# Kernel optimization log

Measured on AMD Instinct MI355X. Metric: run time of the kernel, lower is better.

The kernel has to match this reference:

```python
import jax, jax.numpy as jnp
import numpy as np

B = 512          # number of (query, corpus) pairs
MAX_SET = 128    # max_set_size
D_IN, E_IN = 32, 16
D = 128          # node_state_dim == filters_3
E_ENC = 64
M_HID = 256
T_DIM = 128      # transform_dim
N_PROP = 5
SINKHORN_ITERS = 20
TEMP = 0.1
DEG = 8


def setup_inputs() -> dict:
    key = jax.random.key(0)
    ks = jax.random.split(key, 16)
    # alternating graph sizes: query 128/64, corpus 64/128
    qsizes = np.where(np.arange(B) % 2 == 0, 128, 64).astype(np.int32)
    csizes = np.where(np.arange(B) % 2 == 0, 64, 128).astype(np.int32)
    sizes_flat = np.stack([qsizes, csizes], 1).reshape(-1)        # [2B] interleaved q,c
    N = int(sizes_flat.sum())                                     # 98304
    E = DEG * N                                                   # 786432
    starts = np.concatenate([[0], np.cumsum(sizes_flat)[:-1]])
    graph_idx = np.repeat(np.arange(2 * B), sizes_flat).astype(np.int32)
    rng = np.random.default_rng(0)
    from_idx = rng.integers(0, N, E).astype(np.int64)
    g = graph_idx[from_idx]                                       # keep edges within a graph
    to_idx = (starts[g] + rng.integers(0, 1 << 30, E) % sizes_flat[g]).astype(np.int64)

    def W(k, shape):
        s = 1.0 / np.sqrt(shape[0])
        return jax.random.uniform(k, shape, jnp.float32, -s, s)

    return dict(
        node_features=jax.random.normal(ks[0], (N, D_IN), jnp.float32),
        edge_features=jax.random.normal(ks[1], (E, E_IN), jnp.float32),
        enc_node_w=W(ks[2], (D_IN, D)), enc_node_b=jnp.zeros((D,), jnp.float32),
        enc_edge_w=W(ks[3], (E_IN, E_ENC)), enc_edge_b=jnp.zeros((E_ENC,), jnp.float32),
        msg_w1=W(ks[4], (2 * D + E_ENC, M_HID)), msg_b1=jnp.zeros((M_HID,), jnp.float32),
        msg_w2=W(ks[5], (M_HID, D)), msg_b2=jnp.zeros((D,), jnp.float32),
        rmsg_w1=W(ks[6], (2 * D + E_ENC, M_HID)), rmsg_b1=jnp.zeros((M_HID,), jnp.float32),
        rmsg_w2=W(ks[7], (M_HID, D)), rmsg_b2=jnp.zeros((D,), jnp.float32),
        upd_w1=W(ks[8], (2 * D, M_HID)), upd_b1=jnp.zeros((M_HID,), jnp.float32),
        upd_w2=W(ks[9], (M_HID, D)), upd_b2=jnp.zeros((D,), jnp.float32),
        fc1_w=W(ks[10], (D, T_DIM)), fc1_b=jnp.zeros((T_DIM,), jnp.float32),
        fc2_w=W(ks[11], (T_DIM, T_DIM)), fc2_b=jnp.zeros((T_DIM,), jnp.float32),
        from_idx=jnp.asarray(from_idx, jnp.int32),
        to_idx=jnp.asarray(to_idx, jnp.int32),
        graph_idx=jnp.asarray(graph_idx, jnp.int32),
        qsizes=jnp.asarray(qsizes, jnp.int32),
        csizes=jnp.asarray(csizes, jnp.int32),
    )


def _mlp2(x, w1, b1, w2, b2):
    return jax.nn.relu(x @ w1 + b1) @ w2 + b2


def reference(node_features, edge_features, enc_node_w, enc_node_b, enc_edge_w, enc_edge_b,
              msg_w1, msg_b1, msg_w2, msg_b2, rmsg_w1, rmsg_b1, rmsg_w2, rmsg_b2,
              upd_w1, upd_b1, upd_w2, upd_b2, fc1_w, fc1_b, fc2_w, fc2_b,
              from_idx, to_idx, graph_idx, qsizes, csizes):
    N = node_features.shape[0]
    # GraphEncoder: linear MLPs on node / edge features
    h = node_features @ enc_node_w + enc_node_b                   # [N, D]
    e = edge_features @ enc_edge_w + enc_edge_b                   # [E, E_ENC]
    # GraphPropLayer applied n_prop_layers times (shared params)
    for _ in range(N_PROP):
        src, dst = h[from_idx], h[to_idx]
        m = _mlp2(jnp.concatenate([src, dst, e], -1), msg_w1, msg_b1, msg_w2, msg_b2)
        agg = jax.ops.segment_sum(m, to_idx, num_segments=N)
        mr = _mlp2(jnp.concatenate([dst, src, e], -1), rmsg_w1, rmsg_b1, rmsg_w2, rmsg_b2)
        agg = agg + jax.ops.segment_sum(mr, from_idx, num_segments=N)
        h = h + _mlp2(jnp.concatenate([agg, h], -1), upd_w1, upd_b1, upd_w2, upd_b2)
    # split into per-graph chunks and pad to MAX_SET (scatter by (pair, side, position))
    sizes_flat = jnp.stack([qsizes, csizes], 1).reshape(-1)       # [2B]
    starts = jnp.concatenate([jnp.zeros((1,), sizes_flat.dtype), jnp.cumsum(sizes_flat)[:-1]])
    pos = jnp.arange(N, dtype=jnp.int32) - starts[graph_idx]
    pair, side = graph_idx // 2, graph_idx % 2
    stacked = jnp.zeros((B, 2, MAX_SET, D), h.dtype).at[pair, side, pos].set(h)
    stacked_q, stacked_c = stacked[:, 0], stacked[:, 1]           # [B, MAX_SET, D]
    # masked transform
    tq = _mlp2(stacked_q, fc1_w, fc1_b, fc2_w, fc2_b)
    tc = _mlp2(stacked_c, fc1_w, fc1_b, fc2_w, fc2_b)
    ar = jnp.arange(MAX_SET)
    qmask = (ar[None, :] < qsizes[:, None]).astype(h.dtype)[:, :, None]
    cmask = (ar[None, :] < csizes[:, None]).astype(h.dtype)[:, :, None]
    mq, mc = qmask * tq, cmask * tc
    # sinkhorn (noise_factor = 0, temperature = 0.1, 20 iters)
    log_alpha = jnp.einsum('bqd,bcd->bqc', mq, mc) / TEMP         # [B, MAX_SET, MAX_SET]
    for _ in range(SINKHORN_ITERS):
        log_alpha = log_alpha - jax.scipy.special.logsumexp(log_alpha, axis=2, keepdims=True)
        log_alpha = log_alpha - jax.scipy.special.logsumexp(log_alpha, axis=1, keepdims=True)
    plan = jnp.exp(log_alpha)
    # masked residual score
    scores = -jnp.sum(jax.nn.relu(stacked_q - plan @ stacked_c), axis=(1, 2))  # [B]
    return scores
```

## Files before the change

### kernel.cpp

```cpp
#include <hip/hip_runtime.h>

using bf16x8 = __attribute__((ext_vector_type(8))) __bf16;
using u16x8  = __attribute__((ext_vector_type(8))) unsigned short;
using f32x4  = __attribute__((ext_vector_type(4))) float;
using f32x2  = __attribute__((ext_vector_type(2))) float;

#define DEV static __device__ __forceinline__

constexpr int NN = 98304;
constexpr int NE = 786432;
constexpr int NB = 512;

constexpr size_t OFF_HB  = 0;
constexpr size_t OFF_AGG = OFF_HB + (size_t)NN*128*2;
constexpr size_t OFF_TH  = OFF_AGG;
constexpr size_t OFF_TL  = OFF_AGG + (size_t)NN*128*2;
constexpr size_t OFF_W   = OFF_AGG + (size_t)NN*128*4;

constexpr size_t WO_W1TM = 0;
constexpr size_t WO_W1TR = WO_W1TM + (size_t)81920*2;
constexpr size_t WO_W2TM = WO_W1TR + (size_t)81920*2;
constexpr size_t WO_W2TR = WO_W2TM + (size_t)32768*2;
constexpr size_t WO_W1TU = WO_W2TR + (size_t)32768*2;
constexpr size_t WO_W2TU = WO_W1TU + (size_t)65536*2;
constexpr size_t WO_WNT  = WO_W2TU + (size_t)32768*2;
constexpr size_t WO_WETP = WO_WNT  + (size_t)4096*2;
constexpr size_t WO_FC1F = WO_WETP + (size_t)2048*2;
constexpr size_t WO_FC2F = WO_FC1F + (size_t)16384*4;
constexpr size_t WO_BNF  = WO_FC2F + (size_t)16384*4;
constexpr size_t WO_BEF  = WO_BNF + 128*4;
constexpr size_t WO_B1M  = WO_BEF + 64*4;
constexpr size_t WO_B2M  = WO_B1M + 256*4;
constexpr size_t WO_B1R  = WO_B2M + 128*4;
constexpr size_t WO_B2R  = WO_B1R + 256*4;
constexpr size_t WO_B1U  = WO_B2R + 128*4;
constexpr size_t WO_B2U  = WO_B1U + 256*4;
constexpr size_t WO_FC1B = WO_B2U + 128*4;
constexpr size_t WO_FC2B = WO_FC1B + 128*4;
constexpr size_t WO_FLAG = WO_FC2B + 128*4;
constexpr size_t WO_END  = WO_FLAG + 16;

constexpr size_t OFF_HL  = OFF_W + WO_END;
constexpr size_t WS_MINI = OFF_HL;
constexpr size_t WS_FULL = OFF_HL + (size_t)NN*128*2;

constexpr int    SCAN_CHUNKS= NN/256;
constexpr size_t CSR_INTS   = (size_t)2*(NN+1) + (size_t)2*NN + (size_t)2*NE + 768;
constexpr size_t CSR_BYTES  = CSR_INTS*4;
constexpr size_t WS_FULL_G  = WS_FULL + CSR_BYTES;
constexpr size_t WS_MINI_G  = WS_MINI + CSR_BYTES;

DEV unsigned short f2bf(float f){
  unsigned u = __float_as_uint(f);
  u += 0x7fffu + ((u >> 16) & 1u);
  return (unsigned short)(u >> 16);
}
DEV float bf2f(unsigned short s){ return __uint_as_float(((unsigned)s) << 16); }

DEV unsigned short ldbf(const void* p, size_t i, int fl){
  return fl ? ((const unsigned short*)p)[i] : f2bf(((const float*)p)[i]);
}
DEV float ldf(const void* p, size_t i, int fl){
  return fl ? bf2f(((const unsigned short*)p)[i]) : ((const float*)p)[i];
}

DEV f32x4 mfma16(u16x8 a, u16x8 b, f32x4 c){
  bf16x8 A, B;
  __builtin_memcpy(&A, &a, 16);
  __builtin_memcpy(&B, &b, 16);
  return __builtin_amdgcn_mfma_f32_16x16x32_bf16(A, B, c, 0, 0, 0);
}

__global__ void k_dtype(const unsigned short* nf_u16, int* flag){
  if (threadIdx.x != 0 || blockIdx.x != 0) return;
  int sane = 0;
  for (int i = 0; i < 64; ++i){
    unsigned short v = nf_u16[2*i];
    int e = (v >> 7) & 0xFF;
    if (e >= 0x70 && e <= 0x8E) sane++;
  }
  *flag = (sane >= 32) ? 1 : 0;
}

__global__ void k_sent(float* out){
  int i = blockIdx.x*256 + threadIdx.x;
  if (i < NB) out[i] = 10000.f;
}

__global__ void k_canary(void* out, const int* flag){
  int i = blockIdx.x*256 + threadIdx.x;
  if (i < NB){
    if (*flag) ((unsigned short*)out)[i] = (unsigned short)0x4580u;
    else       ((float*)out)[i] = 4096.f;
  }
}

__global__ void k_zero(float* agg){
  f32x4* p = (f32x4*)agg;
  int gtid = blockIdx.x*256 + threadIdx.x;
  for (int i = gtid; i < NN*128/4; i += 786432){
    f32x4 z = {0.f, 0.f, 0.f, 0.f};
    p[i] = z;
  }
}

__global__ void k_prep(
  const void* enc_node_w, const void* enc_node_b,
  const void* enc_edge_w, const void* enc_edge_b,
  const void* msg_w1, const void* msg_b1,
  const void* msg_w2, const void* msg_b2,
  const void* rmsg_w1, const void* rmsg_b1,
  const void* rmsg_w2, const void* rmsg_b2,
  const void* upd_w1, const void* upd_b1,
  const void* upd_w2, const void* upd_b2,
  const void* fc1_w, const void* fc1_b,
  const void* fc2_w, const void* fc2_b,
  char* wsb)
{
  int fl = *(const int*)(wsb + OFF_W + WO_FLAG);
  int i = blockIdx.x*256 + threadIdx.x;
  unsigned short* W1Tm = (unsigned short*)(wsb + OFF_W + WO_W1TM);
  unsigned short* W1Tr = (unsigned short*)(wsb + OFF_W + WO_W1TR);
  unsigned short* W2Tm = (unsigned short*)(wsb + OFF_W + WO_W2TM);
  unsigned short* W2Tr = (unsigned short*)(wsb + OFF_W + WO_W2TR);
  unsigned short* W1Tu = (unsigned short*)(wsb + OFF_W + WO_W1TU);
  unsigned short* W2Tu = (unsigned short*)(wsb + OFF_W + WO_W2TU);
  unsigned short* WnT  = (unsigned short*)(wsb + OFF_W + WO_WNT);
  unsigned short* WeTp = (unsigned short*)(wsb + OFF_W + WO_WETP);
  float* fc1f = (float*)(wsb + OFF_W + WO_FC1F);
  float* fc2f = (float*)(wsb + OFF_W + WO_FC2F);
  float* bnf  = (float*)(wsb + OFF_W + WO_BNF);
  float* bef  = (float*)(wsb + OFF_W + WO_BEF);
  float* b1m  = (float*)(wsb + OFF_W + WO_B1M);
  float* b2m  = (float*)(wsb + OFF_W + WO_B2M);
  float* b1r  = (float*)(wsb + OFF_W + WO_B1R);
  float* b2r  = (float*)(wsb + OFF_W + WO_B2R);
  float* b1u  = (float*)(wsb + OFF_W + WO_B1U);
  float* b2u  = (float*)(wsb + OFF_W + WO_B2U);
  float* f1b  = (float*)(wsb + OFF_W + WO_FC1B);
  float* f2b  = (float*)(wsb + OFF_W + WO_FC2B);

  if (i < 81920){ W1Tm[i] = ldbf(msg_w1,  (size_t)(i%320)*256 + (i/320), fl); return; } i -= 81920;
  if (i < 81920){ W1Tr[i] = ldbf(rmsg_w1, (size_t)(i%320)*256 + (i/320), fl); return; } i -= 81920;
  if (i < 32768){ W2Tm[i] = ldbf(msg_w2,  (size_t)(i%256)*128 + (i/256), fl); return; } i -= 32768;
  if (i < 32768){ W2Tr[i] = ldbf(rmsg_w2, (size_t)(i%256)*128 + (i/256), fl); return; } i -= 32768;
  if (i < 65536){ W1Tu[i] = ldbf(upd_w1,  (size_t)(i%256)*256 + (i/256), fl); return; } i -= 65536;
  if (i < 32768){ W2Tu[i] = ldbf(upd_w2,  (size_t)(i%256)*128 + (i/256), fl); return; } i -= 32768;
  if (i <  4096){ WnT[i]  = ldbf(enc_node_w, (size_t)(i%32)*128 + (i/32), fl); return; } i -= 4096;
  if (i <  2048){ int k = i%32, n = i/32;
                  WeTp[i] = (k<16) ? ldbf(enc_edge_w, (size_t)k*64 + n, fl) : (unsigned short)0; return; } i -= 2048;
  if (i < 16384){ fc1f[i] = ldf(fc1_w, i, fl); return; } i -= 16384;
  if (i < 16384){ fc2f[i] = ldf(fc2_w, i, fl); return; } i -= 16384;
  if (i <   128){ bnf[i] = ldf(enc_node_b, i, fl); return; } i -= 128;
  if (i <    64){ bef[i] = ldf(enc_edge_b, i, fl); return; } i -= 64;
  if (i <   256){ b1m[i] = ldf(msg_b1, i, fl); return; } i -= 256;
  if (i <   128){ b2m[i] = ldf(msg_b2, i, fl); return; } i -= 128;
  if (i <   256){ b1r[i] = ldf(rmsg_b1, i, fl); return; } i -= 256;
  if (i <   128){ b2r[i] = ldf(rmsg_b2, i, fl); return; } i -= 128;
  if (i <   256){ b1u[i] = ldf(upd_b1, i, fl); return; } i -= 256;
  if (i <   128){ b2u[i] = ldf(upd_b2, i, fl); return; } i -= 128;
  if (i <   128){ f1b[i] = ldf(fc1_b, i, fl); return; } i -= 128;
  if (i <   128){ f2b[i] = ldf(fc2_b, i, fl); return; }
}

__global__ void k_csr_zero(int* cur0, int* cur1){
  int i = blockIdx.x*256 + threadIdx.x;
  if (i < NN){ cur0[i] = 0; cur1[i] = 0; }
}
__global__ void k_csr_count(const int* from_idx, const int* to_idx, int* cur0, int* cur1){
  int e = blockIdx.x*256 + threadIdx.x;
  if (e < NE){
    atomicAdd(&cur0[to_idx[e]], 1);
    atomicAdd(&cur1[from_idx[e]], 1);
  }
}
__global__ void k_scan1(const int* cur0, const int* cur1, int* csum){
  __shared__ int red[256];
  int b = blockIdx.x, tid = threadIdx.x;
  const int* c = (b >= SCAN_CHUNKS) ? cur1 : cur0;
  int cb = (b >= SCAN_CHUNKS) ? (b - SCAN_CHUNKS) : b;
  red[tid] = c[cb*256 + tid];
  __syncthreads();
  for (int off = 128; off > 0; off >>= 1){
    if (tid < off) red[tid] += red[tid + off];
    __syncthreads();
  }
  if (tid == 0) csum[b] = red[0];
}
__global__ void k_scan2(int* csum, int* offs0, int* offs1){
  int wv = threadIdx.x >> 6, lane = threadIdx.x & 63;
  if (wv >= 2) return;
  int basei = wv * SCAN_CHUNKS;
  int carry = 0;
  for (int j = 0; j < SCAN_CHUNKS/64; ++j){
    int x = csum[basei + j*64 + lane];
    int s = x;
    for (int off = 1; off < 64; off <<= 1){
      int t = __shfl_up(s, off, 64);
      if (lane >= off) s += t;
    }
    csum[basei + j*64 + lane] = s - x + carry;
    carry += __shfl(s, 63, 64);
  }
  if (lane == 0){
    if (wv == 0) offs0[NN] = carry; else offs1[NN] = carry;
  }
}
__global__ void k_scan3(int* cur0, int* cur1, const int* csum, int* offs0, int* offs1){
  __shared__ int s[256];
  int b = blockIdx.x, tid = threadIdx.x;
  int dir = (b >= SCAN_CHUNKS) ? 1 : 0;
  int cb  = dir ? (b - SCAN_CHUNKS) : b;
  int* c    = dir ? cur1 : cur0;
  int* offs = dir ? offs1 : offs0;
  int v = c[cb*256 + tid];
  s[tid] = v;
  __syncthreads();
  for (int off = 1; off < 256; off <<= 1){
    int t = (tid >= off) ? s[tid - off] : 0;
    __syncthreads();
    s[tid] += t;
    __syncthreads();
  }
  int excl = s[tid] - v + csum[b];
  offs[cb*256 + tid] = excl;
  c[cb*256 + tid] = excl;
}
__global__ void k_csr_fill(const int* from_idx, const int* to_idx,
                           int* cur0, int* cur1, int* ent0, int* ent1){
  int e = blockIdx.x*256 + threadIdx.x;
  if (e < NE){
    int p0 = atomicAdd(&cur0[to_idx[e]], 1);   ent0[p0] = e;
    int p1 = atomicAdd(&cur1[from_idx[e]], 1); ent1[p1] = e;
  }
}

__global__ void __launch_bounds__(256) k_enc_node(
  const void* nf, const unsigned short* wnt, const float* bnf,
  unsigned short* hb, unsigned short* hl, int has_hl, const int* flag)
{
  int fl = *flag;
  const u16x8* wnt8 = (const u16x8*)wnt;
  int tid = threadIdx.x, wv = tid>>6, lane = tid&63, quad = lane>>4, l15 = lane&15;
  int n0 = blockIdx.x*64;
  f32x4 acc[4][2];
  for (int a=0;a<4;a++){ f32x4 z = {0.f,0.f,0.f,0.f}; acc[a][0]=z; acc[a][1]=z; }
  u16x8 av[4], bv[2];
  if (fl){
    const u16x8* nf8 = (const u16x8*)nf;
    for (int mt=0; mt<4; ++mt) av[mt] = nf8[(size_t)(n0 + mt*16 + l15)*4 + quad];
  } else {
    const float* nff = (const float*)nf;
    for (int mt=0; mt<4; ++mt){
      const float* rp = nff + (size_t)(n0 + mt*16 + l15)*32 + quad*8;
      u16x8 v;
      for (int j=0;j<8;j++) v[j] = f2bf(rp[j]);
      av[mt] = v;
    }
  }
  for (int nt=0; nt<2; ++nt) bv[nt] = wnt8[(size_t)(wv*32 + nt*16 + l15)*4 + quad];
  for (int mt=0; mt<4; ++mt)
    for (int nt=0; nt<2; ++nt)
      acc[mt][nt] = mfma16(av[mt], bv[nt], acc[mt][nt]);
  for (int mt=0; mt<4; ++mt)
    for (int nt=0; nt<2; ++nt){
      int n = wv*32 + nt*16 + l15;
      float bias = bnf[n];
      for (int r=0;r<4;r++){
        int m = mt*16 + quad*4 + r;
        float v = acc[mt][nt][r] + bias;
        size_t idx = (size_t)(n0+m)*128 + n;
        unsigned short hi = f2bf(v);
        hb[idx] = hi;
        if (has_hl) hl[idx] = f2bf(v - bf2f(hi));
      }
    }
}

__global__ void __launch_bounds__(256) k_msg(
  const unsigned short* hbg, const void* efg,
  const int* from_idx, const int* to_idx,
  const unsigned short* w1tm, const unsigned short* w1tr,
  const unsigned short* w2tm, const unsigned short* w2tr,
  const unsigned short* wetp, const float* bef,
  const float* b1m, const float* b2m, const float* b1r, const float* b2r,
  float* agg, const int* flag)
{
  __shared__ __align__(16) unsigned short XsB[40*32*8];
  __shared__ __align__(16) unsigned short HsB[32*32*8];
  __shared__ int fromS[32], toS[32];
  int fl = *flag;
  u16x8* Xs = (u16x8*)XsB;
  u16x8* Hs = (u16x8*)HsB;
  const u16x8* hb8   = (const u16x8*)hbg;
  const u16x8* wetp8 = (const u16x8*)wetp;
  const u16x8* w1tm8 = (const u16x8*)w1tm;
  const u16x8* w1tr8 = (const u16x8*)w1tr;
  const u16x8* w2tm8 = (const u16x8*)w2tm;
  const u16x8* w2tr8 = (const u16x8*)w2tr;

  int tid = threadIdx.x;
  int e0 = blockIdx.x*32;
  if (tid < 32) fromS[tid] = from_idx[e0 + tid];
  else if (tid < 64) toS[tid-32] = to_idx[e0 + tid - 32];
  __syncthreads();
  int m = tid & 31, g = tid >> 5;
  int wv = tid>>6, lane = tid&63, quad = lane>>4, l15 = lane&15;
  u16x8 zero8 = {0,0,0,0,0,0,0,0};

  for (int j=0; j<4; ++j){
    int kb = g + 8*j;
    u16x8 v = (kb < 16) ? hb8[(size_t)fromS[m]*16 + kb]
                        : hb8[(size_t)toS[m]*16 + (kb-16)];
    Xs[kb*32 + m] = v;
  }
  {
    f32x4 accE[2];
    for (int a=0;a<2;a++){ f32x4 z = {0.f,0.f,0.f,0.f}; accE[a]=z; }
    u16x8 bvE = wetp8[(size_t)(wv*16 + l15)*4 + quad];
    for (int mt=0; mt<2; ++mt){
      u16x8 avE = zero8;
      if (quad < 2){
        if (fl){
          avE = ((const u16x8*)efg)[(size_t)(e0 + mt*16 + l15)*2 + quad];
        } else {
          const float* ep = (const float*)efg + (size_t)(e0 + mt*16 + l15)*16 + quad*8;
          u16x8 v;
          for (int j=0;j<8;j++) v[j] = f2bf(ep[j]);
          avE = v;
        }
      }
      accE[mt] = mfma16(avE, bvE, accE[mt]);
    }
    int n = wv*16 + l15;
    float bias = bef[n];
    for (int mt=0; mt<2; ++mt)
      for (int r=0;r<4;r++){
        int me = mt*16 + quad*4 + r;
        XsB[((32 + (n>>3))*32 + me)*8 + (n&7)] = f2bf(accE[mt][r] + bias);
      }
  }
  __syncthreads();

  for (int dir=0; dir<2; ++dir){
    const u16x8* W1T = dir ? w1tr8 : w1tm8;
    const u16x8* W2T = dir ? w2tr8 : w2tm8;
    const float* B1  = dir ? b1r : b1m;
    const float* B2  = dir ? b2r : b2m;
    f32x4 acc1[2][4];
    for (int a=0;a<2;a++)
      for (int b=0;b<4;b++){ f32x4 z = {0.f,0.f,0.f,0.f}; acc1[a][b]=z; }
    for (int ks=0; ks<10; ++ks){
      u16x8 bv[4], av[2];
      for (int nt=0; nt<4; ++nt)
        bv[nt] = W1T[(size_t)(wv*64 + nt*16 + l15)*40 + ks*4 + quad];
      int kb = ks*4 + quad;
      int kbm = dir ? (kb < 32 ? (kb ^ 16) : kb) : kb;
      for (int mt=0; mt<2; ++mt)
        av[mt] = Xs[kbm*32 + mt*16 + l15];
      for (int mt=0; mt<2; ++mt)
        for (int nt=0; nt<4; ++nt)
          acc1[mt][nt] = mfma16(av[mt], bv[nt], acc1[mt][nt]);
    }
    __syncthreads();
    for (int mt=0; mt<2; ++mt)
      for (int nt=0; nt<4; ++nt){
        int n = wv*64 + nt*16 + l15;
        float bias = B1[n];
        for (int r=0;r<4;r++){
          int mm = mt*16 + quad*4 + r;
          float v = fmaxf(acc1[mt][nt][r] + bias, 0.f);
          HsB[((n>>3)*32 + mm)*8 + (n&7)] = f2bf(v);
        }
      }
    __syncthreads();
    f32x4 acc2[2][2];
    for (int a=0;a<2;a++)
      for (int b=0;b<2;b++){ f32x4 z = {0.f,0.f,0.f,0.f}; acc2[a][b]=z; }
    for (int ks=0; ks<8; ++ks){
      u16x8 bv[2], av[2];
      for (int nt=0; nt<2; ++nt)
        bv[nt] = W2T[(size_t)(wv*32 + nt*16 + l15)*32 + ks*4 + quad];
      for (int mt=0; mt<2; ++mt)
        av[mt] = Hs[(ks*4 + quad)*32 + mt*16 + l15];
      for (int mt=0; mt<2; ++mt)
        for (int nt=0; nt<2; ++nt)
          acc2[mt][nt] = mfma16(av[mt], bv[nt], acc2[mt][nt]);
    }
    for (int mt=0; mt<2; ++mt)
      for (int nt=0; nt<2; ++nt){
        int n = wv*32 + nt*16 + l15;
        float bias = B2[n];
        for (int r=0;r<4;r++){
          int mm = mt*16 + quad*4 + r;
          int row = dir ? fromS[mm] : toS[mm];
          atomicAdd(agg + (size_t)row*128 + n, acc2[mt][nt][r] + bias);
        }
      }
  }
}

__global__ void __launch_bounds__(1024, 4) k_msg9(
  const unsigned short* hbg, const void* efg,
  const int* from_idx, const int* to_idx, const int* ent,
  const unsigned short* w1tm, const unsigned short* w1tr,
  const unsigned short* w2tm, const unsigned short* w2tr,
  const unsigned short* wetp, const float* bef,
  const float* b1m, const float* b2m, const float* b1r, const float* b2r,
  float* agg, const int* flag)
{
  __shared__ __align__(16) unsigned short XsB[40*128*8];
  __shared__ __align__(16) unsigned short HsB[32*128*8];
  __shared__ int eS[128], fromS[128], toS[128];
  __shared__ int runBeg[129];
  __shared__ int nRunsS;
  int fl = *flag;
  u16x8* Xs = (u16x8*)XsB;
  u16x8* Hs = (u16x8*)HsB;
  const u16x8* hb8   = (const u16x8*)hbg;
  const u16x8* wetp8 = (const u16x8*)wetp;
  const u16x8* w1tm8 = (const u16x8*)w1tm;
  const u16x8* w1tr8 = (const u16x8*)w1tr;
  const u16x8* w2tm8 = (const u16x8*)w2tm;
  const u16x8* w2tr8 = (const u16x8*)w2tr;

  int tid = threadIdx.x;
  int cpx = (int)gridDim.x >> 3;
  int bb = ((int)blockIdx.x & 7) * cpx + ((int)blockIdx.x >> 3);
  int e0 = bb * 128;
  if (tid < 128){
    int e = ent[e0 + tid];
    eS[tid] = e;
    fromS[tid] = from_idx[e];
    toS[tid]   = to_idx[e];
  }
  __syncthreads();
  int w = tid>>6, lane = tid&63, quad = lane>>4, l15 = lane&15;
  u16x8 zero8 = {0,0,0,0,0,0,0,0};

  if (tid == 0){
    int nr = 0;
    for (int mm=0; mm<128; ++mm)
      if (mm==0 || toS[mm]!=toS[mm-1]) runBeg[nr++] = mm;
    runBeg[nr] = 128; nRunsS = nr;
  }
  {
    int edge = tid & 127, cg = tid >> 7;
    for (int j=0; j<4; ++j){
      int kb = cg + 8*j;
      u16x8 v = (kb < 16) ? hb8[(size_t)fromS[edge]*16 + kb]
                          : hb8[(size_t)toS[edge]*16 + (kb-16)];
      Xs[kb*128 + edge] = v;
    }
  }
  {
    int wm = w >> 2, wn = w & 3;
    f32x4 accE[2];
    for (int a=0;a<2;a++){ f32x4 z = {0.f,0.f,0.f,0.f}; accE[a]=z; }
    u16x8 bvE = wetp8[(size_t)(wn*16 + l15)*4 + quad];
    for (int mt=0; mt<2; ++mt){
      u16x8 avE = zero8;
      if (quad < 2){
        int e = eS[wm*32 + mt*16 + l15];
        if (fl){
          avE = ((const u16x8*)efg)[(size_t)e*2 + quad];
        } else {
          const float* ep = (const float*)efg + (size_t)e*16 + quad*8;
          u16x8 v;
          for (int j=0;j<8;j++) v[j] = f2bf(ep[j]);
          avE = v;
        }
      }
      accE[mt] = mfma16(avE, bvE, accE[mt]);
    }
    int n = wn*16 + l15;
    float bias = bef[n];
    for (int mt=0; mt<2; ++mt)
      for (int r=0;r<4;r++){
        int me = wm*32 + mt*16 + quad*4 + r;
        XsB[((32 + (n>>3))*128 + me)*8 + (n&7)] = f2bf(accE[mt][r] + bias);
      }
  }
  __syncthreads();

  for (int dir=0; dir<2; ++dir){
    const u16x8* W1T = dir ? w1tr8 : w1tm8;
    const u16x8* W2T = dir ? w2tr8 : w2tm8;
    const float* B1  = dir ? b1r : b1m;
    f32x4 acc1[8];
    for (int a=0;a<8;a++){ f32x4 z = {0.f,0.f,0.f,0.f}; acc1[a]=z; }
    int n1 = w*16 + l15;
    for (int ks=0; ks<10; ++ks){
      u16x8 bv1 = W1T[(size_t)n1*40 + ks*4 + quad];
      int kb = ks*4 + quad;
      int kbm = dir ? (kb < 32 ? (kb ^ 16) : kb) : kb;
      u16x8 av[8];
      for (int mt=0; mt<8; ++mt)
        av[mt] = Xs[kbm*128 + mt*16 + l15];
      for (int mt=0; mt<8; ++mt)
        acc1[mt] = mfma16(av[mt], bv1, acc1[mt]);
    }
    if (dir == 1) __syncthreads();
    {
      float bias1 = B1[n1];
      for (int mt=0; mt<8; ++mt)
        for (int r=0;r<4;r++){
          int mm = mt*16 + quad*4 + r;
          float v = fmaxf(acc1[mt][r] + bias1, 0.f);
          HsB[((n1>>3)*128 + mm)*8 + (n1&7)] = f2bf(v);
        }
    }
    __syncthreads();
    int wm2 = w >> 3, wn2 = w & 7;
    int n2 = wn2*16 + l15;
    f32x4 acc2[4];
    for (int a=0;a<4;a++){ f32x4 z = {0.f,0.f,0.f,0.f}; acc2[a]=z; }
    for (int ks=0; ks<8; ++ks){
      u16x8 bv2 = W2T[(size_t)n2*32 + ks*4 + quad];
      u16x8 av[4];
      for (int mt=0; mt<4; ++mt)
        av[mt] = Hs[(ks*4 + quad)*128 + wm2*64 + mt*16 + l15];
      for (int mt=0; mt<4; ++mt)
        acc2[mt] = mfma16(av[mt], bv2, acc2[mt]);
    }
    if (dir == 0){
      __syncthreads();
      float* P = (float*)HsB;
      float bias = b2m[n2];
      for (int mt=0; mt<4; ++mt)
        for (int r=0;r<4;r++){
          int mm = wm2*64 + mt*16 + quad*4 + r;
          P[mm*128 + n2] = acc2[mt][r] + bias;
        }
      __syncthreads();
      int col = tid & 127, grp = tid >> 7;
      int nr = nRunsS;
      for (int k = grp; k < nr; k += 8){
        int r0 = runBeg[k], r1 = runBeg[k+1];
        float s = 0.f;
        for (int mm = r0; mm < r1; ++mm) s += P[mm*128 + col];
        atomicAdd(agg + (size_t)toS[r0]*128 + col, s);
      }
    } else {
      float bias = b2r[n2];
      for (int mt=0; mt<4; ++mt)
        for (int r=0;r<4;r++){
          int mm = wm2*64 + mt*16 + quad*4 + r;
          atomicAdd(agg + (size_t)fromS[mm]*128 + n2, acc2[mt][r] + bias);
        }
    }
  }
}

__global__ void __launch_bounds__(512, 4) k_upd(
  const float* agg, const unsigned short* hbg,
  const unsigned short* w1tu, const unsigned short* w2tu,
  const float* b1u, const float* b2u,
  unsigned short* hb, unsigned short* hl, int has_hl)
{
  __shared__ __align__(16) unsigned short XsB[32*64*8];
  __shared__ __align__(16) unsigned short HsB[32*64*8];
  u16x8* Xs = (u16x8*)XsB;
  u16x8* Hs = (u16x8*)HsB;
  const u16x8* hb8   = (const u16x8*)hbg;
  const u16x8* w1tu8 = (const u16x8*)w1tu;
  const u16x8* w2tu8 = (const u16x8*)w2tu;
  int tid = threadIdx.x;
  int n0 = blockIdx.x*64;
  {
    int node = tid & 63, cg = tid >> 6;
    for (int j=0; j<4; ++j){
      int kb = cg + 8*j;
      u16x8 v;
      if (kb < 16){
        const float* ap = agg + (size_t)(n0+node)*128 + kb*8;
        for (int t=0;t<8;t++) v[t] = f2bf(ap[t]);
      } else {
        v = hb8[(size_t)(n0+node)*16 + (kb-16)];
      }
      Xs[kb*64 + node] = v;
    }
  }
  __syncthreads();
  int w = tid>>6, lane = tid&63, quad = lane>>4, l15 = lane&15;
  f32x4 acc1[4][2];
  for (int a=0;a<4;a++)
    for (int b=0;b<2;b++){ f32x4 z = {0.f,0.f,0.f,0.f}; acc1[a][b]=z; }
  for (int ks=0; ks<8; ++ks){
    u16x8 bv[2], av[4];
    for (int nt=0; nt<2; ++nt)
      bv[nt] = w1tu8[(size_t)(w*32 + nt*16 + l15)*32 + ks*4 + quad];
    for (int mt=0; mt<4; ++mt)
      av[mt] = Xs[(ks*4 + quad)*64 + mt*16 + l15];
    for (int mt=0; mt<4; ++mt)
      for (int nt=0; nt<2; ++nt)
        acc1[mt][nt] = mfma16(av[mt], bv[nt], acc1[mt][nt]);
  }
  __syncthreads();
  for (int mt=0; mt<4; ++mt)
    for (int nt=0; nt<2; ++nt){
      int n = w*32 + nt*16 + l15;
      float bias = b1u[n];
      for (int r=0;r<4;r++){
        int mm = mt*16 + quad*4 + r;
        float v = fmaxf(acc1[mt][nt][r] + bias, 0.f);
        HsB[((n>>3)*64 + mm)*8 + (n&7)] = f2bf(v);
      }
    }
  __syncthreads();
  f32x4 acc2[4];
  for (int a=0;a<4;a++){ f32x4 z = {0.f,0.f,0.f,0.f}; acc2[a]=z; }
  int n2 = w*16 + l15;
  for (int ks=0; ks<8; ++ks){
    u16x8 bv2 = w2tu8[(size_t)n2*32 + ks*4 + quad];
    u16x8 av[4];
    for (int mt=0; mt<4; ++mt)
      av[mt] = Hs[(ks*4 + quad)*64 + mt*16 + l15];
    for (int mt=0; mt<4; ++mt)
      acc2[mt] = mfma16(av[mt], bv2, acc2[mt]);
  }
  float bias = b2u[n2];
  for (int mt=0; mt<4; ++mt)
    for (int r=0;r<4;r++){
      int mm = mt*16 + quad*4 + r;
      size_t idx = (size_t)(n0+mm)*128 + n2;
      float base = bf2f(hb[idx]);
      if (has_hl) base += bf2f(hl[idx]);
      float nv = base + acc2[mt][r] + bias;
      unsigned short hi = f2bf(nv);
      hb[idx] = hi;
      if (has_hl) hl[idx] = f2bf(nv - bf2f(hi));
    }
}

__global__ void __launch_bounds__(256) k_tmlp(
  const unsigned short* hb, const unsigned short* hl, int has_hl,
  const float* fc1f, const float* fc2f,
  const float* fc1b, const float* fc2b, unsigned short* Th, unsigned short* Tl)
{
  __shared__ float Xs[16][128];
  __shared__ float Hsm[16][128];
  int tid = threadIdx.x, wv = tid>>6, lane = tid&63;
  int nodeBase = blockIdx.x*16 + wv*4;
  for (int i=0;i<4;i++){
    size_t base = (size_t)(nodeBase+i)*128 + lane*2;
    float x0 = bf2f(hb[base]), x1 = bf2f(hb[base+1]);
    if (has_hl){ x0 += bf2f(hl[base]); x1 += bf2f(hl[base+1]); }
    Xs[wv*4+i][lane*2] = x0; Xs[wv*4+i][lane*2+1] = x1;
  }
  __syncthreads();
  float a0[4], a1[4];
  for (int i=0;i<4;i++){ a0[i] = fc1b[lane*2]; a1[i] = fc1b[lane*2+1]; }
  for (int k=0;k<128;k++){
    f32x2 w = *(const f32x2*)&fc1f[k*128 + lane*2];
    for (int i=0;i<4;i++){ float x = Xs[wv*4+i][k]; a0[i] += x*w[0]; a1[i] += x*w[1]; }
  }
  for (int i=0;i<4;i++){
    Hsm[wv*4+i][lane*2]   = fmaxf(a0[i], 0.f);
    Hsm[wv*4+i][lane*2+1] = fmaxf(a1[i], 0.f);
  }
  __syncthreads();
  for (int i=0;i<4;i++){ a0[i] = fc2b[lane*2]; a1[i] = fc2b[lane*2+1]; }
  for (int k=0;k<128;k++){
    f32x2 w = *(const f32x2*)&fc2f[k*128 + lane*2];
    for (int i=0;i<4;i++){ float x = Hsm[wv*4+i][k]; a0[i] += x*w[0]; a1[i] += x*w[1]; }
  }
  for (int i=0;i<4;i++){
    size_t idx = (size_t)(nodeBase+i)*128 + lane*2;
    float t0 = a0[i], t1 = a1[i];
    unsigned short h0 = f2bf(t0), h1 = f2bf(t1);
    Th[idx] = h0; Th[idx+1] = h1;
    Tl[idx]   = f2bf(t0 - bf2f(h0));
    Tl[idx+1] = f2bf(t1 - bf2f(h1));
  }
}

__global__ void __launch_bounds__(256) k_pair(
  const unsigned short* Th, const unsigned short* Tl,
  const unsigned short* hb, const unsigned short* hl, int has_hl,
  void* outv, const int* flag)
{
  __shared__ float la[8448];
  __shared__ float red[4];
  const u16x8* th8 = (const u16x8*)Th;
  const u16x8* tl8 = (const u16x8*)Tl;
  int b = blockIdx.x;
  int even = ((b & 1) == 0);
  int qs = even ? 128 : 64;
  int cs = 192 - qs;
  int nr = even ? 128 : 65;
  int nc = even ? 65 : 128;
  int st = nc + 1;
  int q0 = 192*b, c0 = q0 + qs;
  int tid = threadIdx.x, wv = tid>>6, lane = tid&63, quad = lane>>4, l15 = lane&15;
  u16x8 zero8 = {0,0,0,0,0,0,0,0};

  f32x4 acc[2][8];
  for (int a=0;a<2;a++)
    for (int c=0;c<8;c++){ f32x4 z = {0.f,0.f,0.f,0.f}; acc[a][c]=z; }
  for (int pass=0; pass<3; ++pass){
    const u16x8* A  = (pass==2) ? tl8 : th8;
    const u16x8* Bm = (pass==1) ? tl8 : th8;
    for (int ks=0; ks<4; ++ks){
      u16x8 av[2], bv[8];
      for (int mt=0; mt<2; ++mt){
        int q = wv*32 + mt*16 + l15;
        av[mt] = (q < qs) ? A[(size_t)(q0+q)*16 + ks*4 + quad] : zero8;
      }
      for (int nt=0; nt<8; ++nt){
        int c = nt*16 + l15;
        bv[nt] = (c < cs) ? Bm[(size_t)(c0+c)*16 + ks*4 + quad] : zero8;
      }
      for (int mt=0; mt<2; ++mt)
        for (int nt=0; nt<8; ++nt)
          acc[mt][nt] = mfma16(av[mt], bv[nt], acc[mt][nt]);
    }
  }
  for (int mt=0; mt<2; ++mt)
    for (int nt=0; nt<8; ++nt)
      for (int r=0;r<4;r++){
        int q = wv*32 + mt*16 + quad*4 + r;
        int c = nt*16 + l15;
        if (q < nr && c < nc) la[q*st + c] = acc[mt][nt][r] * 10.0f;
      }
  __syncthreads();

  for (int it=0; it<20; ++it){
    if (tid < nr){
      float* row = &la[tid*st];
      float mx = -1e30f;
      for (int c=0;c<nc;c++) mx = fmaxf(mx, row[c]);
      float s = 0.f, last = 0.f;
      for (int c=0;c<nc;c++){ float e = __expf(row[c]-mx); s += e; last = e; }
      if (even) s += 63.f * last;
      float l = mx + __logf(s);
      for (int c=0;c<nc;c++) row[c] -= l;
    }
    __syncthreads();
    if (tid < nc){
      int c = tid;
      float mx = -1e30f;
      for (int r=0;r<nr;r++) mx = fmaxf(mx, la[r*st + c]);
      float s = 0.f, last = 0.f;
      for (int r=0;r<nr;r++){ float e = __expf(la[r*st + c]-mx); s += e; last = e; }
      if (!even) s += 63.f * last;
      float l = mx + __logf(s);
      for (int r=0;r<nr;r++) la[r*st + c] -= l;
    }
    __syncthreads();
  }
  for (int i = tid; i < 8448; i += 256) la[i] = __expf(la[i]);
  __syncthreads();

  int d = tid & 127, qg = tid >> 7;
  int nsweep = (nr + 15) >> 4;
  float partial = 0.f;
  for (int sweep=0; sweep<nsweep; ++sweep){
    int qb = sweep*16 + qg*8;
    float acc2[8];
    for (int j=0;j<8;j++) acc2[j] = 0.f;
    for (int c=0; c<cs; ++c){
      size_t si = (size_t)(c0+c)*128 + d;
      float s = bf2f(hb[si]);
      if (has_hl) s += bf2f(hl[si]);
      for (int j=0;j<8;j++){
        int r = qb + j;
        if (r < nr) acc2[j] += la[r*st + c] * s;
      }
    }
    for (int j=0;j<8;j++){
      int r = qb + j;
      if (r < nr){
        float w = (!even && r == 64) ? 64.f : 1.f;
        float sq = 0.f;
        if (r < qs){
          size_t si = (size_t)(q0+r)*128 + d;
          sq = bf2f(hb[si]);
          if (has_hl) sq += bf2f(hl[si]);
        }
        partial += w * fmaxf(sq - acc2[j], 0.f);
      }
    }
  }
  for (int off=32; off>0; off>>=1) partial += __shfl_down(partial, off, 64);
  if (lane == 0) red[wv] = partial;
  __syncthreads();
  if (tid == 0){
    float tot = red[0] + red[1] + red[2] + red[3];
    if (*flag) ((unsigned short*)outv)[b] = f2bf(-tot);
    else       ((float*)outv)[b] = -tot;
  }
}

extern "C" void kernel_launch(void* const* d_in, const int* in_sizes, int n_in,
                              void* d_out, int out_size, void* d_ws, size_t ws_size,
                              hipStream_t stream)
{
  if (ws_size < WS_MINI){
    k_sent<<<2, 256, 0, stream>>>((float*)d_out);
    return;
  }
  int has_hl = 0, use_s9 = 0;
  size_t off_csr = 0;
  if (ws_size >= WS_FULL_G){ has_hl = 1; use_s9 = 1; off_csr = WS_FULL; }
  else if (ws_size >= WS_FULL){ has_hl = 1; use_s9 = 0; }
  else if (ws_size >= WS_MINI_G){ has_hl = 0; use_s9 = 1; off_csr = WS_MINI; }

  const int* from_idx = (const int*)d_in[22];
  const int* to_idx   = (const int*)d_in[23];

  char* wsb = (char*)d_ws;
  unsigned short* hb  = (unsigned short*)(wsb + OFF_HB);
  unsigned short* hl  = (unsigned short*)(wsb + OFF_HL);
  float* agg          = (float*)(wsb + OFF_AGG);
  unsigned short* Th  = (unsigned short*)(wsb + OFF_TH);
  unsigned short* Tl  = (unsigned short*)(wsb + OFF_TL);
  int* flag           = (int*)(wsb + OFF_W + WO_FLAG);

  const unsigned short* w1tm = (const unsigned short*)(wsb + OFF_W + WO_W1TM);
  const unsigned short* w1tr = (const unsigned short*)(wsb + OFF_W + WO_W1TR);
  const unsigned short* w2tm = (const unsigned short*)(wsb + OFF_W + WO_W2TM);
  const unsigned short* w2tr = (const unsigned short*)(wsb + OFF_W + WO_W2TR);
  const unsigned short* w1tu = (const unsigned short*)(wsb + OFF_W + WO_W1TU);
  const unsigned short* w2tu = (const unsigned short*)(wsb + OFF_W + WO_W2TU);
  const unsigned short* wnt  = (const unsigned short*)(wsb + OFF_W + WO_WNT);
  const unsigned short* wetp = (const unsigned short*)(wsb + OFF_W + WO_WETP);
  const float* fc1f  = (const float*)(wsb + OFF_W + WO_FC1F);
  const float* fc2f  = (const float*)(wsb + OFF_W + WO_FC2F);
  const float* bnf   = (const float*)(wsb + OFF_W + WO_BNF);
  const float* bef   = (const float*)(wsb + OFF_W + WO_BEF);
  const float* b1m   = (const float*)(wsb + OFF_W + WO_B1M);
  const float* b2m   = (const float*)(wsb + OFF_W + WO_B2M);
  const float* b1r   = (const float*)(wsb + OFF_W + WO_B1R);
  const float* b2r   = (const float*)(wsb + OFF_W + WO_B2R);
  const float* b1u   = (const float*)(wsb + OFF_W + WO_B1U);
  const float* b2u   = (const float*)(wsb + OFF_W + WO_B2U);
  const float* f1b   = (const float*)(wsb + OFF_W + WO_FC1B);
  const float* f2b   = (const float*)(wsb + OFF_W + WO_FC2B);

  int* offs0 = (int*)(wsb + off_csr);
  int* offs1 = offs0 + (NN + 1);
  int* cur0  = offs1 + (NN + 1);
  int* cur1  = cur0 + NN;
  int* ent0  = cur1 + NN;
  int* ent1  = ent0 + NE;
  int* csum  = ent1 + NE;

  k_dtype<<<1, 64, 0, stream>>>((const unsigned short*)d_in[0], flag);

  k_canary<<<2, 256, 0, stream>>>(d_out, flag);

  k_prep<<<1439, 256, 0, stream>>>(
    d_in[2],  d_in[3],  d_in[4],  d_in[5],
    d_in[6],  d_in[7],  d_in[8],  d_in[9],
    d_in[10], d_in[11], d_in[12], d_in[13],
    d_in[14], d_in[15], d_in[16], d_in[17],
    d_in[18], d_in[19], d_in[20], d_in[21],
    wsb);

  if (use_s9){
    k_csr_zero <<<NN/256, 256, 0, stream>>>(cur0, cur1);
    k_csr_count<<<NE/256, 256, 0, stream>>>(from_idx, to_idx, cur0, cur1);
    k_scan1    <<<2*SCAN_CHUNKS, 256, 0, stream>>>(cur0, cur1, csum);
    k_scan2    <<<1, 128, 0, stream>>>(csum, offs0, offs1);
    k_scan3    <<<2*SCAN_CHUNKS, 256, 0, stream>>>(cur0, cur1, csum, offs0, offs1);
    k_csr_fill <<<NE/256, 256, 0, stream>>>(from_idx, to_idx, cur0, cur1, ent0, ent1);
  }

  k_enc_node<<<NN/64, 256, 0, stream>>>(d_in[0], wnt, bnf, hb, hl, has_hl, flag);

  for (int r=0; r<5; ++r){
    k_zero<<<3072, 256, 0, stream>>>(agg);
    if (use_s9){
      k_msg9<<<NE/128, 1024, 0, stream>>>(hb, d_in[1],
          from_idx, to_idx, ent0, w1tm, w1tr, w2tm, w2tr, wetp, bef,
          b1m, b2m, b1r, b2r, agg, flag);
    } else {
      k_msg<<<NE/32, 256, 0, stream>>>(hb, d_in[1],
          from_idx, to_idx, w1tm, w1tr, w2tm, w2tr, wetp, bef,
          b1m, b2m, b1r, b2r, agg, flag);
    }
    k_upd<<<NN/64, 512, 0, stream>>>(agg, hb, w1tu, w2tu, b1u, b2u, hb, hl, has_hl);
  }

  k_tmlp<<<NN/16, 256, 0, stream>>>(hb, hl, has_hl, fc1f, fc2f, f1b, f2b, Th, Tl);
  k_pair<<<NB, 256, 0, stream>>>(Th, Tl, hb, hl, has_hl, d_out, flag);
}
```

Baseline: 6.004 ms.

## Shrink message kernel tile to 64 edges, prefetch weights, fuse agg zeroing into update

The message kernel now processes 64 edges per 512-thread block instead of 128 per 1024-thread block. Each wave computes a 32-column slice of the first GEMM, which halves LDS use and allows more resident blocks. The weight B-fragments in the message and update GEMMs are register double-buffered, loading the next k-step while the current MFMAs issue. The per-round k_zero launch is dropped: k_upd clears its own agg rows after reading them, so only one initial zero pass remains. The trade-offs are larger edge-segment run overhead from smaller tiles and more atomics per edge group, and the in-place zeroing relies on each block owning its agg rows.

```diff
diff --git a/kernel.cpp b/kernel.cpp
--- a/kernel.cpp
+++ b/kernel.cpp
@@ -400,7 +400,7 @@
   }
 }
 
-__global__ void __launch_bounds__(1024, 4) k_msg9(
+__global__ void __launch_bounds__(512, 4) k_msg8(
   const unsigned short* hbg, const void* efg,
   const int* from_idx, const int* to_idx, const int* ent,
   const unsigned short* w1tm, const unsigned short* w1tr,
@@ -409,10 +409,10 @@
   const float* b1m, const float* b2m, const float* b1r, const float* b2r,
   float* agg, const int* flag)
 {
-  __shared__ __align__(16) unsigned short XsB[40*128*8];
-  __shared__ __align__(16) unsigned short HsB[32*128*8];
-  __shared__ int eS[128], fromS[128], toS[128];
-  __shared__ int runBeg[129];
+  __shared__ __align__(16) unsigned short XsB[40*64*8];
+  __shared__ __align__(16) unsigned short HsB[32*64*8];
+  __shared__ int eS[64], fromS[64], toS[64];
+  __shared__ int runBeg[65];
   __shared__ int nRunsS;
   int fl = *flag;
   u16x8* Xs = (u16x8*)XsB;
@@ -427,8 +427,8 @@
   int tid = threadIdx.x;
   int cpx = (int)gridDim.x >> 3;
   int bb = ((int)blockIdx.x & 7) * cpx + ((int)blockIdx.x >> 3);
-  int e0 = bb * 128;
-  if (tid < 128){
+  int e0 = bb * 64;
+  if (tid < 64){
     int e = ent[e0 + tid];
     eS[tid] = e;
     fromS[tid] = from_idx[e];
@@ -440,17 +440,17 @@
 
   if (tid == 0){
     int nr = 0;
-    for (int mm=0; mm<128; ++mm)
+    for (int mm=0; mm<64; ++mm)
       if (mm==0 || toS[mm]!=toS[mm-1]) runBeg[nr++] = mm;
-    runBeg[nr] = 128; nRunsS = nr;
+    runBeg[nr] = 64; nRunsS = nr;
   }
   {
-    int edge = tid & 127, cg = tid >> 7;
+    int edge = tid & 63, cg = tid >> 6;
     for (int j=0; j<4; ++j){
       int kb = cg + 8*j;
       u16x8 v = (kb < 16) ? hb8[(size_t)fromS[edge]*16 + kb]
                           : hb8[(size_t)toS[edge]*16 + (kb-16)];
-      Xs[kb*128 + edge] = v;
+      Xs[kb*64 + edge] = v;
     }
   }
   {
@@ -478,7 +478,7 @@
     for (int mt=0; mt<2; ++mt)
       for (int r=0;r<4;r++){
         int me = wm*32 + mt*16 + quad*4 + r;
-        XsB[((32 + (n>>3))*128 + me)*8 + (n&7)] = f2bf(accE[mt][r] + bias);
+        XsB[((32 + (n>>3))*64 + me)*8 + (n&7)] = f2bf(accE[mt][r] + bias);
       }
   }
   __syncthreads();
@@ -487,41 +487,52 @@
     const u16x8* W1T = dir ? w1tr8 : w1tm8;
     const u16x8* W2T = dir ? w2tr8 : w2tm8;
     const float* B1  = dir ? b1r : b1m;
-    f32x4 acc1[8];
-    for (int a=0;a<8;a++){ f32x4 z = {0.f,0.f,0.f,0.f}; acc1[a]=z; }
-    int n1 = w*16 + l15;
+    f32x4 acc1[4][2];
+    for (int a=0;a<4;a++)
+      for (int b=0;b<2;b++){ f32x4 z = {0.f,0.f,0.f,0.f}; acc1[a][b]=z; }
+    u16x8 bvA[2], bvB[2];
+    for (int nt=0; nt<2; ++nt)
+      bvA[nt] = W1T[(size_t)(w*32 + nt*16 + l15)*40 + quad];
     for (int ks=0; ks<10; ++ks){
-      u16x8 bv1 = W1T[(size_t)n1*40 + ks*4 + quad];
+      if (ks < 9)
+        for (int nt=0; nt<2; ++nt)
+          bvB[nt] = W1T[(size_t)(w*32 + nt*16 + l15)*40 + (ks+1)*4 + quad];
+      else { bvB[0] = bvA[0]; bvB[1] = bvA[1]; }
       int kb = ks*4 + quad;
       int kbm = dir ? (kb < 32 ? (kb ^ 16) : kb) : kb;
-      u16x8 av[8];
-      for (int mt=0; mt<8; ++mt)
-        av[mt] = Xs[kbm*128 + mt*16 + l15];
-      for (int mt=0; mt<8; ++mt)
-        acc1[mt] = mfma16(av[mt], bv1, acc1[mt]);
+      u16x8 av[4];
+      for (int mt=0; mt<4; ++mt)
+        av[mt] = Xs[kbm*64 + mt*16 + l15];
+      for (int mt=0; mt<4; ++mt)
+        for (int nt=0; nt<2; ++nt)
+          acc1[mt][nt] = mfma16(av[mt], bvA[nt], acc1[mt][nt]);
+      bvA[0] = bvB[0]; bvA[1] = bvB[1];
     }
     if (dir == 1) __syncthreads();
-    {
-      float bias1 = B1[n1];
-      for (int mt=0; mt<8; ++mt)
+    for (int mt=0; mt<4; ++mt)
+      for (int nt=0; nt<2; ++nt){
+        int n = w*32 + nt*16 + l15;
+        float bias = B1[n];
         for (int r=0;r<4;r++){
           int mm = mt*16 + quad*4 + r;
-          float v = fmaxf(acc1[mt][r] + bias1, 0.f);
-          HsB[((n1>>3)*128 + mm)*8 + (n1&7)] = f2bf(v);
+          float v = fmaxf(acc1[mt][nt][r] + bias, 0.f);
+          HsB[((n>>3)*64 + mm)*8 + (n&7)] = f2bf(v);
         }
-    }
+      }
     __syncthreads();
-    int wm2 = w >> 3, wn2 = w & 7;
-    int n2 = wn2*16 + l15;
     f32x4 acc2[4];
     for (int a=0;a<4;a++){ f32x4 z = {0.f,0.f,0.f,0.f}; acc2[a]=z; }
+    int n2 = w*16 + l15;
+    u16x8 bvC = W2T[(size_t)n2*32 + quad];
     for (int ks=0; ks<8; ++ks){
-      u16x8 bv2 = W2T[(size_t)n2*32 + ks*4 + quad];
+      u16x8 bvN = bvC;
+      if (ks < 7) bvN = W2T[(size_t)n2*32 + (ks+1)*4 + quad];
       u16x8 av[4];
       for (int mt=0; mt<4; ++mt)
-        av[mt] = Hs[(ks*4 + quad)*128 + wm2*64 + mt*16 + l15];
+        av[mt] = Hs[(ks*4 + quad)*64 + mt*16 + l15];
       for (int mt=0; mt<4; ++mt)
-        acc2[mt] = mfma16(av[mt], bv2, acc2[mt]);
+        acc2[mt] = mfma16(av[mt], bvC, acc2[mt]);
+      bvC = bvN;
     }
     if (dir == 0){
       __syncthreads();
@@ -529,13 +540,13 @@
       float bias = b2m[n2];
       for (int mt=0; mt<4; ++mt)
         for (int r=0;r<4;r++){
-          int mm = wm2*64 + mt*16 + quad*4 + r;
+          int mm = mt*16 + quad*4 + r;
           P[mm*128 + n2] = acc2[mt][r] + bias;
         }
       __syncthreads();
       int col = tid & 127, grp = tid >> 7;
       int nr = nRunsS;
-      for (int k = grp; k < nr; k += 8){
+      for (int k = grp; k < nr; k += 4){
         int r0 = runBeg[k], r1 = runBeg[k+1];
         float s = 0.f;
         for (int mm = r0; mm < r1; ++mm) s += P[mm*128 + col];
@@ -545,7 +556,7 @@
       float bias = b2r[n2];
       for (int mt=0; mt<4; ++mt)
         for (int r=0;r<4;r++){
-          int mm = wm2*64 + mt*16 + quad*4 + r;
+          int mm = mt*16 + quad*4 + r;
           atomicAdd(agg + (size_t)fromS[mm]*128 + n2, acc2[mt][r] + bias);
         }
     }
@@ -553,7 +564,7 @@
 }
 
 __global__ void __launch_bounds__(512, 4) k_upd(
-  const float* agg, const unsigned short* hbg,
+  float* agg, const unsigned short* hbg,
   const unsigned short* w1tu, const unsigned short* w2tu,
   const float* b1u, const float* b2u,
   unsigned short* hb, unsigned short* hl, int has_hl)
@@ -582,19 +593,32 @@
     }
   }
   __syncthreads();
+  {
+    f32x4* ap4 = (f32x4*)(agg + (size_t)n0*128);
+    f32x4 z = {0.f,0.f,0.f,0.f};
+    for (int i = tid; i < 64*128/4; i += 512) ap4[i] = z;
+  }
   int w = tid>>6, lane = tid&63, quad = lane>>4, l15 = lane&15;
   f32x4 acc1[4][2];
   for (int a=0;a<4;a++)
     for (int b=0;b<2;b++){ f32x4 z = {0.f,0.f,0.f,0.f}; acc1[a][b]=z; }
-  for (int ks=0; ks<8; ++ks){
-    u16x8 bv[2], av[4];
+  {
+    u16x8 bvA[2], bvB[2];
     for (int nt=0; nt<2; ++nt)
-      bv[nt] = w1tu8[(size_t)(w*32 + nt*16 + l15)*32 + ks*4 + quad];
-    for (int mt=0; mt<4; ++mt)
-      av[mt] = Xs[(ks*4 + quad)*64 + mt*16 + l15];
-    for (int mt=0; mt<4; ++mt)
-      for (int nt=0; nt<2; ++nt)
-        acc1[mt][nt] = mfma16(av[mt], bv[nt], acc1[mt][nt]);
+      bvA[nt] = w1tu8[(size_t)(w*32 + nt*16 + l15)*32 + quad];
+    for (int ks=0; ks<8; ++ks){
+      if (ks < 7)
+        for (int nt=0; nt<2; ++nt)
+          bvB[nt] = w1tu8[(size_t)(w*32 + nt*16 + l15)*32 + (ks+1)*4 + quad];
+      else { bvB[0] = bvA[0]; bvB[1] = bvA[1]; }
+      u16x8 av[4];
+      for (int mt=0; mt<4; ++mt)
+        av[mt] = Xs[(ks*4 + quad)*64 + mt*16 + l15];
+      for (int mt=0; mt<4; ++mt)
+        for (int nt=0; nt<2; ++nt)
+          acc1[mt][nt] = mfma16(av[mt], bvA[nt], acc1[mt][nt]);
+      bvA[0] = bvB[0]; bvA[1] = bvB[1];
+    }
   }
   __syncthreads();
   for (int mt=0; mt<4; ++mt)
@@ -611,13 +635,18 @@
   f32x4 acc2[4];
   for (int a=0;a<4;a++){ f32x4 z = {0.f,0.f,0.f,0.f}; acc2[a]=z; }
   int n2 = w*16 + l15;
-  for (int ks=0; ks<8; ++ks){
-    u16x8 bv2 = w2tu8[(size_t)n2*32 + ks*4 + quad];
-    u16x8 av[4];
-    for (int mt=0; mt<4; ++mt)
-      av[mt] = Hs[(ks*4 + quad)*64 + mt*16 + l15];
-    for (int mt=0; mt<4; ++mt)
-      acc2[mt] = mfma16(av[mt], bv2, acc2[mt]);
+  {
+    u16x8 bvC = w2tu8[(size_t)n2*32 + quad];
+    for (int ks=0; ks<8; ++ks){
+      u16x8 bvN = bvC;
+      if (ks < 7) bvN = w2tu8[(size_t)n2*32 + (ks+1)*4 + quad];
+      u16x8 av[4];
+      for (int mt=0; mt<4; ++mt)
+        av[mt] = Hs[(ks*4 + quad)*64 + mt*16 + l15];
+      for (int mt=0; mt<4; ++mt)
+        acc2[mt] = mfma16(av[mt], bvC, acc2[mt]);
+      bvC = bvN;
+    }
   }
   float bias = b2u[n2];
   for (int mt=0; mt<4; ++mt)
@@ -800,11 +829,11 @@
     k_sent<<<2, 256, 0, stream>>>((float*)d_out);
     return;
   }
-  int has_hl = 0, use_s9 = 0;
+  int has_hl = 0, use_s8 = 0;
   size_t off_csr = 0;
-  if (ws_size >= WS_FULL_G){ has_hl = 1; use_s9 = 1; off_csr = WS_FULL; }
-  else if (ws_size >= WS_FULL){ has_hl = 1; use_s9 = 0; }
-  else if (ws_size >= WS_MINI_G){ has_hl = 0; use_s9 = 1; off_csr = WS_MINI; }
+  if (ws_size >= WS_FULL_G){ has_hl = 1; use_s8 = 1; off_csr = WS_FULL; }
+  else if (ws_size >= WS_FULL){ has_hl = 1; use_s8 = 0; }
+  else if (ws_size >= WS_MINI_G){ has_hl = 0; use_s8 = 1; off_csr = WS_MINI; }
 
   const int* from_idx = (const int*)d_in[22];
   const int* to_idx   = (const int*)d_in[23];
@@ -858,7 +887,7 @@
     d_in[18], d_in[19], d_in[20], d_in[21],
     wsb);
 
-  if (use_s9){
+  if (use_s8){
     k_csr_zero <<<NN/256, 256, 0, stream>>>(cur0, cur1);
     k_csr_count<<<NE/256, 256, 0, stream>>>(from_idx, to_idx, cur0, cur1);
     k_scan1    <<<2*SCAN_CHUNKS, 256, 0, stream>>>(cur0, cur1, csum);
@@ -869,10 +898,10 @@
 
   k_enc_node<<<NN/64, 256, 0, stream>>>(d_in[0], wnt, bnf, hb, hl, has_hl, flag);
 
+  k_zero<<<3072, 256, 0, stream>>>(agg);
   for (int r=0; r<5; ++r){
-    k_zero<<<3072, 256, 0, stream>>>(agg);
-    if (use_s9){
-      k_msg9<<<NE/128, 1024, 0, stream>>>(hb, d_in[1],
+    if (use_s8){
+      k_msg8<<<NE/64, 512, 0, stream>>>(hb, d_in[1],
           from_idx, to_idx, ent0, w1tm, w1tr, w2tm, w2tr, wetp, bef,
           b1m, b2m, b1r, b2r, agg, flag);
     } else {
```

Result: faster. 5.816 ms (-3.1%).
